# Kernel tuning notes

Measured on AMD Instinct MI355X. Metric: run time of the kernel, lower is better.

The kernel has to match this reference:

```python
import jax, jax.numpy as jnp
import numpy as np

N_NODES = 20000  # number of atoms (scatter target count)


def setup_inputs() -> dict:
    key = jax.random.key(0)
    ks = jax.random.split(key, 7)
    E, F, R, L, O = 640000, 128, 16, 3, 12
    return {
        "m_ji": jax.random.normal(ks[0], (E, F), jnp.float32),
        "rbf_ji": jax.random.normal(ks[1], (E, R), jnp.float32),
        "atom_edge_index": jax.random.randint(ks[2], (2, E), 0, N_NODES, jnp.int64),
        "W_rbf": jax.random.normal(ks[3], (F, R), jnp.float32) * (1.0 / np.sqrt(R)),
        "dense_W": jax.random.normal(ks[4], (L, F, F), jnp.float32) * (1.0 / np.sqrt(F)),
        "dense_b": jax.random.normal(ks[5], (L, F), jnp.float32) * 0.01,
        "W_out": jax.random.normal(ks[6], (O, F), jnp.float32) * (1.0 / np.sqrt(F)),
    }


def reference(m_ji, rbf_ji, atom_edge_index, W_rbf, dense_W, dense_b, W_out):
    # e_ji = lin_rbf(rbf_ji): [E, dim_rbf] @ [dim_rbf, F] -> [E, F]
    e_ji = jnp.einsum("er,fr->ef", rbf_ji, W_rbf)
    # elementwise gate
    message_ji = e_ji * m_ji
    # scatter-add messages onto receiving atoms (index row 1)
    atom_i = jax.ops.segment_sum(message_ji, atom_edge_index[1], num_segments=N_NODES)
    # dense MLP stack with SiLU activation
    num_lin = dense_W.shape[0]
    for idx in range(num_lin):
        atom_i = jax.nn.silu(jnp.einsum("nf,gf->ng", atom_i, dense_W[idx]) + dense_b[idx])
    # final bias-free projection
    return jnp.einsum("nf,of->no", atom_i, W_out)
```

## Files before the change

### kernel.cpp

```cpp
#include <hip/hip_runtime.h>
#include <math.h>

#define F 128
#define R 16
#define O 12
#define NB 32

__global__ void zero_int_kernel(int* __restrict__ p, int n) {
    int i = blockIdx.x * blockDim.x + threadIdx.x;
    if (i < n) p[i] = 0;
}

__global__ __launch_bounds__(256) void hist_kernel(
    const int* __restrict__ idx, int* __restrict__ cnt, int E)
{
    int i = blockIdx.x * blockDim.x + threadIdx.x;
    int stride = gridDim.x * blockDim.x;
    for (; i < E; i += stride) atomicAdd(&cnt[idx[i]], 1);
}

__global__ __launch_bounds__(1024) void scan_kernel(
    const int* __restrict__ cnt, int* __restrict__ off,
    int* __restrict__ cur, int N, int E)
{
    __shared__ int part[1024];
    int t = threadIdx.x;
    const int per = (N + 1023) / 1024;
    int s0 = t * per;
    int s = 0;
    for (int i = 0; i < per; i++) { int k = s0 + i; if (k < N) s += cnt[k]; }
    part[t] = s;
    __syncthreads();
    for (int d = 1; d < 1024; d <<= 1) {
        int v = (t >= d) ? part[t - d] : 0;
        __syncthreads();
        part[t] += v;
        __syncthreads();
    }
    int run = (t == 0) ? 0 : part[t - 1];
    for (int i = 0; i < per; i++) {
        int k = s0 + i;
        if (k < N) { off[k] = run; cur[k] = run; run += cnt[k]; }
    }
    if (t == 0) off[N] = E;
}

__global__ __launch_bounds__(256) void fill_kernel(
    const int* __restrict__ idx, int* __restrict__ cur,
    int* __restrict__ csr, int E)
{
    int i = blockIdx.x * blockDim.x + threadIdx.x;
    int stride = gridDim.x * blockDim.x;
    for (; i < E; i += stride) {
        int n = idx[i];
        int p = atomicAdd(&cur[n], 1);
        csr[p] = i;
    }
}

__device__ __forceinline__ float dot16(const float4* r, const float4* Wv) {
    float s = 0.f;
    #pragma unroll
    for (int q = 0; q < 4; q++)
        s += r[q].x * Wv[q].x + r[q].y * Wv[q].y + r[q].z * Wv[q].z + r[q].w * Wv[q].w;
    return s;
}

__global__ __launch_bounds__(256) void gather_kernel(
    const float* __restrict__ m, const float* __restrict__ rbf,
    const int* __restrict__ csr, const int* __restrict__ off,
    const float* __restrict__ Wrbf, float* __restrict__ A, int N)
{
    int lane = threadIdx.x & 63;
    int w = threadIdx.x >> 6;
    int n = blockIdx.x * 4 + w;
    if (n >= N) return;

    int f0 = lane << 1;
    float4 W0[4], W1[4];
    #pragma unroll
    for (int q = 0; q < 4; q++) {
        W0[q] = *(const float4*)(Wrbf + (size_t)f0 * R + q * 4);
        W1[q] = *(const float4*)(Wrbf + (size_t)(f0 + 1) * R + q * 4);
    }

    float a0 = 0.f, a1 = 0.f;
    int jb = off[n], je = off[n + 1];

    int j = jb;
    for (; j + 4 <= je; j += 4) {
        int e0 = csr[j];
        int e1 = csr[j + 1];
        int e2 = csr[j + 2];
        int e3 = csr[j + 3];
        float2 m0 = *(const float2*)(m + (size_t)e0 * F + f0);
        float2 m1 = *(const float2*)(m + (size_t)e1 * F + f0);
        float2 m2 = *(const float2*)(m + (size_t)e2 * F + f0);
        float2 m3 = *(const float2*)(m + (size_t)e3 * F + f0);
        float4 r0[4], r1[4], r2[4], r3[4];
        #pragma unroll
        for (int q = 0; q < 4; q++) {
            r0[q] = ((const float4*)(rbf + (size_t)e0 * R))[q];
            r1[q] = ((const float4*)(rbf + (size_t)e1 * R))[q];
            r2[q] = ((const float4*)(rbf + (size_t)e2 * R))[q];
            r3[q] = ((const float4*)(rbf + (size_t)e3 * R))[q];
        }
        a0 += dot16(r0, W0) * m0.x;  a1 += dot16(r0, W1) * m0.y;
        a0 += dot16(r1, W0) * m1.x;  a1 += dot16(r1, W1) * m1.y;
        a0 += dot16(r2, W0) * m2.x;  a1 += dot16(r2, W1) * m2.y;
        a0 += dot16(r3, W0) * m3.x;  a1 += dot16(r3, W1) * m3.y;
    }
    for (; j < je; j++) {
        int e0 = csr[j];
        float2 m0 = *(const float2*)(m + (size_t)e0 * F + f0);
        float4 r0[4];
        #pragma unroll
        for (int q = 0; q < 4; q++)
            r0[q] = ((const float4*)(rbf + (size_t)e0 * R))[q];
        a0 += dot16(r0, W0) * m0.x;
        a1 += dot16(r0, W1) * m0.y;
    }

    *(float2*)(A + (size_t)n * F + f0) = make_float2(a0, a1);
}

__global__ __launch_bounds__(256) void mlp_fused(
    const float* __restrict__ A, const float* __restrict__ dW,
    const float* __restrict__ db, const float* __restrict__ Wout,
    float* __restrict__ out, int N)
{
    __shared__ float Ws[F * F];
    __shared__ float act[NB * F];
    int t = threadIdx.x;
    int base = blockIdx.x * NB;
    int j = t & 15, i = t >> 4;

    int  n0[2]; bool ok[2];
    #pragma unroll
    for (int k = 0; k < 2; k++) { n0[k] = base + i + 16 * k; ok[k] = n0[k] < N; }

    for (int l = 0; l < 3; l++) {
        __syncthreads();
        for (int s = t; s < F * F / 4; s += 256) {
            int g = s >> 5, c = s & 31;
            float4 v = *(const float4*)(dW + (size_t)l * F * F + g * F + (c << 2));
            *(float4*)(Ws + g * F + ((c ^ (g & 31)) << 2)) = v;
        }
        __syncthreads();

        float acc[2][8];
        #pragma unroll
        for (int k = 0; k < 2; k++)
            #pragma unroll
            for (int mm = 0; mm < 8; mm++) acc[k][mm] = 0.f;

        for (int c = 0; c < 32; c++) {
            int f = c << 2;
            float4 av[2];
            #pragma unroll
            for (int k = 0; k < 2; k++) {
                if (l == 0)
                    av[k] = ok[k] ? *(const float4*)(A + (size_t)n0[k] * F + f)
                                  : make_float4(0.f, 0.f, 0.f, 0.f);
                else
                    av[k] = *(const float4*)(act + (i + 16 * k) * F + f);
            }
            float4 wv[8];
            #pragma unroll
            for (int mm = 0; mm < 8; mm++) {
                int g = j + 16 * mm;
                wv[mm] = *(const float4*)(Ws + g * F + ((c ^ (g & 31)) << 2));
            }
            #pragma unroll
            for (int k = 0; k < 2; k++)
                #pragma unroll
                for (int mm = 0; mm < 8; mm++)
                    acc[k][mm] += av[k].x * wv[mm].x + av[k].y * wv[mm].y +
                                  av[k].z * wv[mm].z + av[k].w * wv[mm].w;
        }

        #pragma unroll
        for (int mm = 0; mm < 8; mm++) {
            int g = j + 16 * mm;
            float bias = db[l * F + g];
            #pragma unroll
            for (int k = 0; k < 2; k++) {
                float x = acc[k][mm] + bias;
                act[(i + 16 * k) * F + g] = x / (1.f + __expf(-x));
            }
        }
    }

    __syncthreads();
    for (int s = t; s < O * F / 4; s += 256)
        ((float4*)Ws)[s] = ((const float4*)Wout)[s];
    __syncthreads();

    int nl = t >> 3;
    int oq = t & 7;
    int n = base + nl;
    if (n < N) {
        float s0 = 0.f, s1 = 0.f;
        for (int f = 0; f < F; f += 4) {
            float4 a  = *(const float4*)(act + nl * F + f);
            float4 w0 = *(const float4*)(Ws + oq * F + f);
            s0 += a.x * w0.x + a.y * w0.y + a.z * w0.z + a.w * w0.w;
            if (oq < 4) {
                float4 w1 = *(const float4*)(Ws + (8 + oq) * F + f);
                s1 += a.x * w1.x + a.y * w1.y + a.z * w1.z + a.w * w1.w;
            }
        }
        out[(size_t)n * O + oq] = s0;
        if (oq < 4) out[(size_t)n * O + 8 + oq] = s1;
    }
}

extern "C" void kernel_launch(void* const* d_in, const int* in_sizes, int n_in,
                              void* d_out, int out_size, void* d_ws, size_t ws_size,
                              hipStream_t stream)
{
    const float* m    = (const float*)d_in[0];
    const float* rbf  = (const float*)d_in[1];
    const int*   aei  = (const int*)d_in[2];
    const float* Wrbf = (const float*)d_in[3];
    const float* dW   = (const float*)d_in[4];
    const float* db   = (const float*)d_in[5];
    const float* Wout = (const float*)d_in[6];
    float* out = (float*)d_out;

    int E = in_sizes[0] / F;
    int N = out_size / O;

    float* A = (float*)d_ws;
    int* csr = (int*)(A + (size_t)N * F);
    int* cnt = csr + E;
    int* cur = cnt + N;
    int* off = cur + N;

    const int* idx1 = aei + E;

    zero_int_kernel<<<(N + 255) / 256, 256, 0, stream>>>(cnt, N);
    hist_kernel<<<1024, 256, 0, stream>>>(idx1, cnt, E);
    scan_kernel<<<1, 1024, 0, stream>>>(cnt, off, cur, N, E);
    fill_kernel<<<1024, 256, 0, stream>>>(idx1, cur, csr, E);
    gather_kernel<<<(N + 3) / 4, 256, 0, stream>>>(m, rbf, csr, off, Wrbf, A, N);

    mlp_fused<<<(N + NB - 1) / NB, 256, 0, stream>>>(A, dW, db, Wout, out, N);
}
```

Baseline: 784.5 us.

## Split each node's edge list across two wavefronts with prefetched CSR indices

The gather kernel now assigns two wavefronts to each destination node. Each wavefront handles half of the node's edges, and the partial sums are combined through shared memory. The CSR index loads for the next group of four edges are prefetched ahead of use, and a scheduling barrier keeps the loads ahead of the FMAs. Launch bounds request higher occupancy. The goal is more memory-level parallelism and shorter per-wave serial chains, at the cost of a block-wide sync and an LDS reduction.

```diff
diff --git a/kernel.cpp b/kernel.cpp
--- a/kernel.cpp
+++ b/kernel.cpp
@@ -66,17 +66,20 @@
     return s;
 }
 
-__global__ __launch_bounds__(256) void gather_kernel(
+__global__ __launch_bounds__(256, 4) void gather_kernel(
     const float* __restrict__ m, const float* __restrict__ rbf,
     const int* __restrict__ csr, const int* __restrict__ off,
     const float* __restrict__ Wrbf, float* __restrict__ A, int N)
 {
-    int lane = threadIdx.x & 63;
-    int w = threadIdx.x >> 6;
-    int n = blockIdx.x * 4 + w;
-    if (n >= N) return;
-
-    int f0 = lane << 1;
+    __shared__ float part[2 * F];
+    const int lane = threadIdx.x & 63;
+    const int w    = threadIdx.x >> 6;
+    const int ln   = w >> 1;
+    const int half = w & 1;
+    const int n = blockIdx.x * 2 + ln;
+    const bool active = (n < N);
+
+    const int f0 = lane << 1;
     float4 W0[4], W1[4];
     #pragma unroll
     for (int q = 0; q < 4; q++) {
@@ -85,43 +88,64 @@
     }
 
     float a0 = 0.f, a1 = 0.f;
-    int jb = off[n], je = off[n + 1];
-
-    int j = jb;
-    for (; j + 4 <= je; j += 4) {
-        int e0 = csr[j];
-        int e1 = csr[j + 1];
-        int e2 = csr[j + 2];
-        int e3 = csr[j + 3];
-        float2 m0 = *(const float2*)(m + (size_t)e0 * F + f0);
-        float2 m1 = *(const float2*)(m + (size_t)e1 * F + f0);
-        float2 m2 = *(const float2*)(m + (size_t)e2 * F + f0);
-        float2 m3 = *(const float2*)(m + (size_t)e3 * F + f0);
-        float4 r0[4], r1[4], r2[4], r3[4];
-        #pragma unroll
-        for (int q = 0; q < 4; q++) {
-            r0[q] = ((const float4*)(rbf + (size_t)e0 * R))[q];
-            r1[q] = ((const float4*)(rbf + (size_t)e1 * R))[q];
-            r2[q] = ((const float4*)(rbf + (size_t)e2 * R))[q];
-            r3[q] = ((const float4*)(rbf + (size_t)e3 * R))[q];
-        }
-        a0 += dot16(r0, W0) * m0.x;  a1 += dot16(r0, W1) * m0.y;
-        a0 += dot16(r1, W0) * m1.x;  a1 += dot16(r1, W1) * m1.y;
-        a0 += dot16(r2, W0) * m2.x;  a1 += dot16(r2, W1) * m2.y;
-        a0 += dot16(r3, W0) * m3.x;  a1 += dot16(r3, W1) * m3.y;
-    }
-    for (; j < je; j++) {
-        int e0 = csr[j];
-        float2 m0 = *(const float2*)(m + (size_t)e0 * F + f0);
-        float4 r0[4];
-        #pragma unroll
-        for (int q = 0; q < 4; q++)
-            r0[q] = ((const float4*)(rbf + (size_t)e0 * R))[q];
-        a0 += dot16(r0, W0) * m0.x;
-        a1 += dot16(r0, W1) * m0.y;
-    }
-
-    *(float2*)(A + (size_t)n * F + f0) = make_float2(a0, a1);
+
+    if (active) {
+        const int jb = off[n], je = off[n + 1];
+        const int cnt = je - jb;
+        const int c0 = (cnt >> 1) & ~3;
+        int j       = half ? (jb + c0) : jb;
+        const int e = half ? je        : (jb + c0);
+
+        if (j + 4 <= e) {
+            int e0 = csr[j], e1 = csr[j + 1], e2 = csr[j + 2], e3 = csr[j + 3];
+            while (j + 4 <= e) {
+                const int jn = j + 4;
+                const int jp = (jn + 4 <= e) ? jn : j;
+                int p0 = csr[jp], p1 = csr[jp + 1], p2 = csr[jp + 2], p3 = csr[jp + 3];
+
+                float2 m0 = *(const float2*)(m + (size_t)e0 * F + f0);
+                float2 m1 = *(const float2*)(m + (size_t)e1 * F + f0);
+                float2 m2 = *(const float2*)(m + (size_t)e2 * F + f0);
+                float2 m3 = *(const float2*)(m + (size_t)e3 * F + f0);
+                float4 r0[4], r1[4], r2[4], r3[4];
+                #pragma unroll
+                for (int q = 0; q < 4; q++) {
+                    r0[q] = ((const float4*)(rbf + (size_t)e0 * R))[q];
+                    r1[q] = ((const float4*)(rbf + (size_t)e1 * R))[q];
+                    r2[q] = ((const float4*)(rbf + (size_t)e2 * R))[q];
+                    r3[q] = ((const float4*)(rbf + (size_t)e3 * R))[q];
+                }
+                __builtin_amdgcn_sched_barrier(0);
+                a0 += dot16(r0, W0) * m0.x;  a1 += dot16(r0, W1) * m0.y;
+                a0 += dot16(r1, W0) * m1.x;  a1 += dot16(r1, W1) * m1.y;
+                a0 += dot16(r2, W0) * m2.x;  a1 += dot16(r2, W1) * m2.y;
+                a0 += dot16(r3, W0) * m3.x;  a1 += dot16(r3, W1) * m3.y;
+                e0 = p0; e1 = p1; e2 = p2; e3 = p3;
+                j = jn;
+            }
+        }
+        for (; j < e; j++) {
+            const int e0 = csr[j];
+            float2 m0 = *(const float2*)(m + (size_t)e0 * F + f0);
+            float4 r0[4];
+            #pragma unroll
+            for (int q = 0; q < 4; q++)
+                r0[q] = ((const float4*)(rbf + (size_t)e0 * R))[q];
+            a0 += dot16(r0, W0) * m0.x;
+            a1 += dot16(r0, W1) * m0.y;
+        }
+    }
+
+    if (half == 1) {
+        part[ln * F + f0]     = a0;
+        part[ln * F + f0 + 1] = a1;
+    }
+    __syncthreads();
+    if (active && half == 0) {
+        a0 += part[ln * F + f0];
+        a1 += part[ln * F + f0 + 1];
+        *(float2*)(A + (size_t)n * F + f0) = make_float2(a0, a1);
+    }
 }
 
 __global__ __launch_bounds__(256) void mlp_fused(
@@ -243,7 +267,7 @@
     hist_kernel<<<1024, 256, 0, stream>>>(idx1, cnt, E);
     scan_kernel<<<1, 1024, 0, stream>>>(cnt, off, cur, N, E);
     fill_kernel<<<1024, 256, 0, stream>>>(idx1, cur, csr, E);
-    gather_kernel<<<(N + 3) / 4, 256, 0, stream>>>(m, rbf, csr, off, Wrbf, A, N);
+    gather_kernel<<<(N + 1) / 2, 256, 0, stream>>>(m, rbf, csr, off, Wrbf, A, N);
 
     mlp_fused<<<(N + NB - 1) / NB, 256, 0, stream>>>(A, dW, db, Wout, out, N);
 }
```

Result: slower. 886.8 us (+13.0%).

## Stage gathered edge rows into LDS via global_load_lds in gather kernel

Applied to the files above, without the earlier changes.

The gather kernel now loads chunks of 16 edges' m and rbf rows directly into per-wave LDS buffers using the async global_load_lds builtin, then accumulates from LDS. Each chunk issues full 16-byte loads per lane, covering 2 edges of m per instruction, instead of scattered float2/float4 register loads. This aims to raise memory-level parallelism and coalescing in the bandwidth-bound gather. It adds LDS traffic, a full vmcnt wait per chunk with no double buffering, and it relies on the LDS write layout of the builtin matching the indexing used afterwards.

```diff
diff --git a/kernel.cpp b/kernel.cpp
--- a/kernel.cpp
+++ b/kernel.cpp
@@ -5,6 +5,7 @@
 #define R 16
 #define O 12
 #define NB 32
+#define EB 16
 
 __global__ void zero_int_kernel(int* __restrict__ p, int n) {
     int i = blockIdx.x * blockDim.x + threadIdx.x;
@@ -66,17 +67,29 @@
     return s;
 }
 
+__device__ __forceinline__ void gld_lds16(const float* g, float* l) {
+    __builtin_amdgcn_global_load_lds(
+        (const __attribute__((address_space(1))) void*)g,
+        (__attribute__((address_space(3))) void*)l,
+        16, 0, 0);
+}
+
 __global__ __launch_bounds__(256) void gather_kernel(
     const float* __restrict__ m, const float* __restrict__ rbf,
     const int* __restrict__ csr, const int* __restrict__ off,
     const float* __restrict__ Wrbf, float* __restrict__ A, int N)
 {
-    int lane = threadIdx.x & 63;
-    int w = threadIdx.x >> 6;
-    int n = blockIdx.x * 4 + w;
+    __shared__ float m_buf[4 * EB * F];
+    __shared__ float r_buf[4 * EB * R];
+    const int lane = threadIdx.x & 63;
+    const int w = threadIdx.x >> 6;
+    const int n = blockIdx.x * 4 + w;
     if (n >= N) return;
 
-    int f0 = lane << 1;
+    float* mw = m_buf + w * EB * F;
+    float* rw = r_buf + w * EB * R;
+
+    const int f0 = lane << 1;
     float4 W0[4], W1[4];
     #pragma unroll
     for (int q = 0; q < 4; q++) {
@@ -85,40 +98,38 @@
     }
 
     float a0 = 0.f, a1 = 0.f;
-    int jb = off[n], je = off[n + 1];
-
-    int j = jb;
-    for (; j + 4 <= je; j += 4) {
-        int e0 = csr[j];
-        int e1 = csr[j + 1];
-        int e2 = csr[j + 2];
-        int e3 = csr[j + 3];
-        float2 m0 = *(const float2*)(m + (size_t)e0 * F + f0);
-        float2 m1 = *(const float2*)(m + (size_t)e1 * F + f0);
-        float2 m2 = *(const float2*)(m + (size_t)e2 * F + f0);
-        float2 m3 = *(const float2*)(m + (size_t)e3 * F + f0);
-        float4 r0[4], r1[4], r2[4], r3[4];
+    const int jb = off[n], je = off[n + 1];
+
+    for (int j = jb; j < je; j += EB) {
+        const int c = (je - j < EB) ? (je - j) : EB;
+
+        asm volatile("s_waitcnt lgkmcnt(0)" ::: "memory");
+
         #pragma unroll
-        for (int q = 0; q < 4; q++) {
-            r0[q] = ((const float4*)(rbf + (size_t)e0 * R))[q];
-            r1[q] = ((const float4*)(rbf + (size_t)e1 * R))[q];
-            r2[q] = ((const float4*)(rbf + (size_t)e2 * R))[q];
-            r3[q] = ((const float4*)(rbf + (size_t)e3 * R))[q];
-        }
-        a0 += dot16(r0, W0) * m0.x;  a1 += dot16(r0, W1) * m0.y;
-        a0 += dot16(r1, W0) * m1.x;  a1 += dot16(r1, W1) * m1.y;
-        a0 += dot16(r2, W0) * m2.x;  a1 += dot16(r2, W1) * m2.y;
-        a0 += dot16(r3, W0) * m3.x;  a1 += dot16(r3, W1) * m3.y;
-    }
-    for (; j < je; j++) {
-        int e0 = csr[j];
-        float2 m0 = *(const float2*)(m + (size_t)e0 * F + f0);
-        float4 r0[4];
-        #pragma unroll
-        for (int q = 0; q < 4; q++)
-            r0[q] = ((const float4*)(rbf + (size_t)e0 * R))[q];
-        a0 += dot16(r0, W0) * m0.x;
-        a1 += dot16(r0, W1) * m0.y;
+        for (int k = 0; k < EB / 2; k++) {
+            if (2 * k < c) {
+                int jj = j + 2 * k + (lane >> 5);
+                if (jj > je - 1) jj = je - 1;
+                int e = csr[jj];
+                gld_lds16(m + (size_t)e * F + ((lane & 31) << 2), mw + k * 2 * F);
+            }
+        }
+        {
+            int jj = j + (lane >> 2);
+            if (jj > je - 1) jj = je - 1;
+            int e = csr[jj];
+            gld_lds16(rbf + (size_t)e * R + ((lane & 3) << 2), rw);
+        }
+
+        asm volatile("s_waitcnt vmcnt(0)" ::: "memory");
+
+        for (int r = 0; r < c; r++) {
+            float2 mv = *(const float2*)(mw + r * F + f0);
+            const float4* rr = (const float4*)(rw + r * R);
+            float4 rv[4] = { rr[0], rr[1], rr[2], rr[3] };
+            a0 += dot16(rv, W0) * mv.x;
+            a1 += dot16(rv, W1) * mv.y;
+        }
     }
 
     *(float2*)(A + (size_t)n * F + f0) = make_float2(a0, a1);
```

After: 743.4 us. 1.06x faster.
